# Performance work log

Hardware: AMD Instinct MI355X
Metric: run time of the kernel (lower is better)

Reference implementation:

```python
import jax, jax.numpy as jnp
import numpy as np

EPS = 1e-8


def setup_inputs() -> dict:
    key = jax.random.key(0)
    x = jax.random.normal(key, (16384, 1024), dtype=jnp.float32)
    return {"x": x}


def reference(x) -> jnp.ndarray:
    # L2 normalize along feature dim (torch F.normalize: x / max(||x||, eps))
    norm = jnp.linalg.norm(x, axis=-1, keepdims=True)
    xn = x / jnp.maximum(norm, EPS)

    n = xn.shape[0]
    # full pairwise cosine similarity [N, N]
    dot = xn @ xn.T
    # mask self-similarity on the diagonal
    ii = jnp.arange(n)
    dot = dot.at[ii, ii].set(-1.0)
    # nearest neighbor per row
    index = jnp.argmax(dot, axis=1)

    # torch PairwiseDistance(p=2, eps=1e-8): ||x1 - x2 + eps||_2
    diff = xn - xn[index] + EPS
    distances = jnp.linalg.norm(diff, axis=-1)

    loss = -jnp.mean(jnp.log(distances + EPS))
    return loss
```

## Files before the change

kernel.cpp:

```cpp
#include <hip/hip_runtime.h>
#include <math.h>

#define N 16384
#define D 1024
#define EPSF 1e-8f
#define QSCALE 448.0f
#define NPAIRS 2080
#define PANB 262144

typedef __attribute__((ext_vector_type(4))) int i32x4;
typedef unsigned int u32;
typedef unsigned long long u64;

#define LDS_Bb 65536
#define LDS_TOT 131088

__device__ __forceinline__ void gload_lds16(const void* g, void* l) {
  __builtin_amdgcn_global_load_lds(
      (const __attribute__((address_space(1))) u32*)g,
      (__attribute__((address_space(3))) u32*)l, 16, 0, 0);
}

__device__ __forceinline__ u64 maxu64(u64 x, u64 y) { return x > y ? x : y; }

__device__ __forceinline__ void decode_pair(int t, int& a, int& b) {
  int aa = (int)((129.0 - sqrt(129.0 * 129.0 - 8.0 * (double)t)) * 0.5);
  if (aa < 0) aa = 0;
  if (aa > 63) aa = 63;
  while (((aa + 1) * 64 - ((aa + 1) * aa) / 2) <= t) ++aa;
  while ((aa * 64 - (aa * (aa - 1)) / 2) > t) --aa;
  a = aa;
  b = aa + (t - (aa * 64 - (aa * (aa - 1)) / 2));
}


__global__ __launch_bounds__(256) void k_normalize(
    const float* __restrict__ x, signed char* __restrict__ xq,
    float* __restrict__ norms, u64* __restrict__ best, int* __restrict__ ctr) {
  const int w = threadIdx.x >> 6, lane = threadIdx.x & 63;
  const int i = blockIdx.x * 4 + w;
  if (threadIdx.x < 4) best[(size_t)blockIdx.x * 4 + threadIdx.x] = 0;
  if (blockIdx.x == 0 && threadIdx.x == 0) *ctr = 0;
  const float4* xi = (const float4*)(x + (size_t)i * D);
  float4 v[4];
  float s = 0.f;
#pragma unroll
  for (int t = 0; t < 4; ++t) {
    v[t] = xi[lane + t * 64];
    s += v[t].x * v[t].x + v[t].y * v[t].y + v[t].z * v[t].z + v[t].w * v[t].w;
  }
#pragma unroll
  for (int sh = 32; sh; sh >>= 1) s += __shfl_xor(s, sh, 64);
  const float nrm = sqrtf(s);
  if (lane == 0) norms[i] = nrm;
  const float qs = QSCALE / fmaxf(nrm, EPSF);
  u32* xo = (u32*)(xq + (size_t)i * D);
#pragma unroll
  for (int t = 0; t < 4; ++t) {
    const int q0 = __float2int_rn(fminf(fmaxf(v[t].x * qs, -127.f), 127.f));
    const int q1 = __float2int_rn(fminf(fmaxf(v[t].y * qs, -127.f), 127.f));
    const int q2 = __float2int_rn(fminf(fmaxf(v[t].z * qs, -127.f), 127.f));
    const int q3 = __float2int_rn(fminf(fmaxf(v[t].w * qs, -127.f), 127.f));
    xo[lane + t * 64] = (u32)(q0 & 0xff) | ((u32)(q1 & 0xff) << 8) |
                        ((u32)(q2 & 0xff) << 16) | ((u32)(q3 & 0xff) << 24);
  }
}


#define SG(gaddr, daddr) \
  gload_lds16(xqB + (gaddr) + srcLane, lds + (daddr) + w * 1024)

#define KT1(K_)                                                                \
  {                                                                            \
    __builtin_amdgcn_s_barrier();                                              \
    asm volatile("" ::: "memory");                                             \
    if ((K_) < 13) {                                                           \
      const size_t aG = aPan + (size_t)(((K_) + 3) * 64);                      \
      const size_t bG = bPan + (size_t)(((K_) + 3) * 64);                      \
      SG(aG, (((K_) + 3) & 3) * 16384);                                        \
      SG(aG + 131072, (((K_) + 3) & 3) * 16384 + 8192);                        \
      SG(bG, LDS_Bb + (((K_) + 3) & 3) * 16384);                               \
      SG(bG + 131072, LDS_Bb + (((K_) + 3) & 3) * 16384 + 8192);               \
    } else if (hasNext) {                                                      \
      const size_t aG = aPanN + (size_t)(((K_)-13) * 64);                      \
      const size_t bG = bPanN + (size_t)(((K_)-13) * 64);                      \
      SG(aG, (((K_) + 3) & 3) * 16384);                                        \
      SG(aG + 131072, (((K_) + 3) & 3) * 16384 + 8192);                        \
      SG(bG, LDS_Bb + (((K_) + 3) & 3) * 16384);                               \
      SG(bG + 131072, LDS_Bb + (((K_) + 3) & 3) * 16384 + 8192);               \
    }                                                                          \
    i32x4 aa[4], bb[4];                                                        \
    _Pragma("unroll") for (int m = 0; m < 4; ++m) aa[m] =                      \
        *(const i32x4*)(lds + ((K_)&3) * 16384 + aOff[m]);                     \
    _Pragma("unroll") for (int n = 0; n < 4; ++n) bb[n] =                      \
        *(const i32x4*)(lds + LDS_Bb + ((K_)&3) * 16384 + bOff[n]);            \
    __builtin_amdgcn_s_setprio(1);                                             \
    _Pragma("unroll") for (int m = 0; m < 4; ++m)                              \
      _Pragma("unroll") for (int n = 0; n < 4; ++n)                            \
        acc[m][n] = __builtin_amdgcn_mfma_i32_16x16x64_i8(aa[m], bb[n],        \
                                                          acc[m][n], 0, 0, 0); \
    __builtin_amdgcn_s_setprio(0);                                             \
    _Pragma("unroll") for (int n = 0; n < 4; ++n) bb[n] =                      \
        *(const i32x4*)(lds + LDS_Bb + ((K_)&3) * 16384 + bOff[4 + n]);        \
    __builtin_amdgcn_s_setprio(1);                                             \
    _Pragma("unroll") for (int m = 0; m < 4; ++m)                              \
      _Pragma("unroll") for (int n = 0; n < 4; ++n)                            \
        acc[m][4 + n] = __builtin_amdgcn_mfma_i32_16x16x64_i8(                 \
            aa[m], bb[n], acc[m][4 + n], 0, 0, 0);                             \
    __builtin_amdgcn_s_setprio(0);                                             \
    asm volatile("s_waitcnt vmcnt(8)" ::: "memory");                           \
  }

__global__ __launch_bounds__(512, 2) void k_argmax(
    const signed char* __restrict__ xq, u64* __restrict__ best,
    int* __restrict__ ctr) {
  extern __shared__ char lds[];
  int* s_next = (int*)(lds + 131072);
  const char* xqB = (const char*)xq;
  const int tid = (int)threadIdx.x, lane = tid & 63, w = tid >> 6;
  const int wr = w >> 1, wc = w & 1;

  int aOff[4], bOff[8];
  const int q = lane >> 4, li = lane & 15;
#pragma unroll
  for (int m = 0; m < 4; ++m) {
    const int rr = wr * 64 + m * 16 + li;
    const int line = rr >> 1;
    aOff[m] = line * 128 + ((((rr & 1) << 6) | (q << 4)) ^ ((line & 7) << 4));
  }
#pragma unroll
  for (int nf = 0; nf < 8; ++nf) {
    const int rr = wc * 128 + nf * 16 + li;
    const int line = rr >> 1;
    bOff[nf] = line * 128 + ((((rr & 1) << 6) | (q << 4)) ^ ((line & 7) << 4));
  }
  const int posx = (lane & 7) ^ (lane >> 3);
  const int rrl = ((w * 8 + (lane >> 3)) << 1) | (posx >> 2);
  const int srcLane = rrl * 1024 + (posx & 3) * 16;

  const int rB2 = wr * 64 + (q << 2);
  const int cB2 = wc * 128 + li;

  if (tid == 0) {
    s_next[0] = atomicAdd(ctr, 1);
    s_next[1] = atomicAdd(ctr, 1);
  }
  __syncthreads();
  int pcur = s_next[0], pnext = s_next[1];
  __syncthreads();
  if (pcur >= NPAIRS) return;

  int a, b;
  decode_pair(pcur, a, b);
  size_t aPan = (size_t)a * PANB, bPan = (size_t)b * PANB;
  for (int p = 0; p < 3; ++p) {
    SG(aPan + (size_t)(p * 64), p * 16384);
    SG(aPan + (size_t)(p * 64) + 131072, p * 16384 + 8192);
    SG(bPan + (size_t)(p * 64), LDS_Bb + p * 16384);
    SG(bPan + (size_t)(p * 64) + 131072, LDS_Bb + p * 16384 + 8192);
  }
  asm volatile("s_waitcnt vmcnt(8)" ::: "memory");

  int par = 0;
  i32x4 acc[4][8];
  while (true) {
    const bool hasNext = (pnext < NPAIRS);
    int an = 0, bn = 0;
    if (hasNext) decode_pair(pnext, an, bn);
    const size_t aPanN = (size_t)an * PANB, bPanN = (size_t)bn * PANB;
    if (tid == 0) s_next[par] = atomicAdd(ctr, 1);

#pragma unroll
    for (int m = 0; m < 4; ++m)
#pragma unroll
      for (int n = 0; n < 8; ++n) acc[m][n] = (i32x4){0, 0, 0, 0};

    KT1(0); KT1(1); KT1(2); KT1(3);
    KT1(4); KT1(5); KT1(6); KT1(7);
    KT1(8); KT1(9); KT1(10); KT1(11);
    KT1(12); KT1(13); KT1(14); KT1(15);

    const int aBase = a * 256, colBase = b * 256;
#pragma unroll
    for (int m = 0; m < 4; ++m)
#pragma unroll
      for (int r = 0; r < 4; ++r) {
        const int rl = rB2 + m * 16 + r;
        int pm = (int)0x80000000;
        if (a == b) {
#pragma unroll
          for (int nf = 0; nf < 8; ++nf) {
            int pv = (int)(((u32)acc[m][nf][r] << 3) | (u32)nf);
            if (rl == cB2 + nf * 16) pv = (int)0x80000000;
            pm = pm > pv ? pm : pv;
          }
        } else {
#pragma unroll
          for (int nf = 0; nf < 8; ++nf) {
            const int pv = (int)(((u32)acc[m][nf][r] << 3) | (u32)nf);
            pm = pm > pv ? pm : pv;
          }
        }
        const u32 mono = (u32)(pm >> 3) ^ 0x80000000u;
        u64 p = ((u64)mono << 32) | (u32)(colBase + cB2 + ((pm & 7) << 4));
#pragma unroll
        for (int sh = 1; sh < 16; sh <<= 1)
          p = maxu64(p, __shfl_xor(p, sh, 64));
        if (li == 0) atomicMax(best + (aBase + rl), p);
      }

    if (a != b) {
#pragma unroll
      for (int nf = 0; nf < 8; ++nf) {
        int pv = (int)0x80000000;
#pragma unroll
        for (int m = 0; m < 4; ++m)
#pragma unroll
          for (int r = 0; r < 4; ++r) {
            const int c =
                (int)(((u32)acc[m][nf][r] << 6) | (u32)(m * 16 + q * 4 + r));
            pv = pv > c ? pv : c;
          }
        {
          const int o1 = __shfl_xor(pv, 16, 64);
          pv = pv > o1 ? pv : o1;
          const int o2 = __shfl_xor(pv, 32, 64);
          pv = pv > o2 ? pv : o2;
        }
        if (q == 0) {
          const int dot = pv >> 6;
          const int grow = aBase + wr * 64 + (pv & 63);
          const u64 pk = ((u64)((u32)dot ^ 0x80000000u) << 32) | (u32)grow;
          atomicMax(best + (colBase + cB2 + nf * 16), pk);
        }
      }
    }

    if (!hasNext) break;
    const int pnn = s_next[par];
    pcur = pnext;
    a = an; b = bn;
    aPan = aPanN; bPan = bPanN;
    pnext = pnn;
    par ^= 1;
  }
}


__global__ __launch_bounds__(256) void k_dist(
    const float* __restrict__ x, const float* __restrict__ norms,
    const u64* __restrict__ best, float* __restrict__ logd) {
  const int w = threadIdx.x >> 6, lane = threadIdx.x & 63;
  const int i = blockIdx.x * 4 + w;
  const u64 p = best[i];
  const int j = (int)(p & 0xffffffffu);
  const float invi = 1.f / fmaxf(norms[i], EPSF);
  const float invj = 1.f / fmaxf(norms[j], EPSF);
  const float4* xi = (const float4*)(x + (size_t)i * D);
  const float4* xj = (const float4*)(x + (size_t)j * D);
  float s = 0.f;
#pragma unroll
  for (int t = 0; t < 4; ++t) {
    const float4 av = xi[lane + t * 64], bv = xj[lane + t * 64];
    float d;
    d = av.x * invi - bv.x * invj + EPSF; s += d * d;
    d = av.y * invi - bv.y * invj + EPSF; s += d * d;
    d = av.z * invi - bv.z * invj + EPSF; s += d * d;
    d = av.w * invi - bv.w * invj + EPSF; s += d * d;
  }
#pragma unroll
  for (int sh = 32; sh; sh >>= 1) s += __shfl_xor(s, sh, 64);
  if (lane == 0) logd[i] = logf(sqrtf(s) + EPSF);
}


__global__ __launch_bounds__(256) void k_final(const float* __restrict__ logd,
                                               float* __restrict__ out) {
  __shared__ double red[256];
  double s = 0.0;
  for (int i = threadIdx.x; i < N; i += 256) s += (double)logd[i];
  red[threadIdx.x] = s;
  __syncthreads();
  for (int sh = 128; sh; sh >>= 1) {
    if ((int)threadIdx.x < sh) red[threadIdx.x] += red[threadIdx.x + sh];
    __syncthreads();
  }
  if (threadIdx.x == 0) out[0] = (float)(-red[0] / (double)N);
}


extern "C" void kernel_launch(void* const* d_in, const int* in_sizes, int n_in,
                              void* d_out, int out_size, void* d_ws,
                              size_t ws_size, hipStream_t stream) {
  const float* x = (const float*)d_in[0];
  float* out = (float*)d_out;
  char* ws = (char*)d_ws;

  signed char* xq = (signed char*)ws;
  float* norms = (float*)(ws + 16777216);
  u64* best = (u64*)(ws + 16842752);
  float* logd = (float*)(ws + 16973824);
  int* ctr = (int*)(ws + 17039360);

  k_normalize<<<N / 4, 256, 0, stream>>>(x, xq, norms, best, ctr);
  k_argmax<<<256, 512, LDS_TOT, stream>>>(xq, best, ctr);
  k_dist<<<N / 4, 256, 0, stream>>>(x, norms, best, logd);
  k_final<<<1, 256, 0, stream>>>(logd, out);
}
```

Measured before the change: 252.9 us.

## Load A operand directly from global via transposed int8 copy, deepen B LDS ring

The normalize kernel now also writes a transposed, MFMA-fragment-ordered copy of the quantized matrix. The argmax kernel reads A fragments straight from global memory into registers instead of staging them through LDS. B alone uses the freed LDS as an 8-slot ring with a 4-tile prefetch distance, and barriers run once per group of four k-tiles with a full vmcnt(0) wait. This cuts LDS traffic and barrier count, at the cost of extra workspace, scattered 4-byte transposed writes in normalize, and global-load latency on A that is exposed directly to the MFMAs.

Measured after the change: 279.1 us. 10.4% more time.

```diff
diff --git a/kernel.cpp b/kernel.cpp
--- a/kernel.cpp
+++ b/kernel.cpp
@@ -7,12 +7,12 @@
 #define QSCALE 448.0f
 #define NPAIRS 2080
 #define PANB 262144
+#define GRANB 262144
 
 typedef __attribute__((ext_vector_type(4))) int i32x4;
 typedef unsigned int u32;
 typedef unsigned long long u64;
 
-#define LDS_Bb 65536
 #define LDS_TOT 131088
 
 __device__ __forceinline__ void gload_lds16(const void* g, void* l) {
@@ -36,7 +36,8 @@
 
 __global__ __launch_bounds__(256) void k_normalize(
     const float* __restrict__ x, signed char* __restrict__ xq,
-    float* __restrict__ norms, u64* __restrict__ best, int* __restrict__ ctr) {
+    signed char* __restrict__ xqT, float* __restrict__ norms,
+    u64* __restrict__ best, int* __restrict__ ctr) {
   const int w = threadIdx.x >> 6, lane = threadIdx.x & 63;
   const int i = blockIdx.x * 4 + w;
   if (threadIdx.x < 4) best[(size_t)blockIdx.x * 4 + threadIdx.x] = 0;
@@ -55,79 +56,95 @@
   if (lane == 0) norms[i] = nrm;
   const float qs = QSCALE / fmaxf(nrm, EPSF);
   u32* xo = (u32*)(xq + (size_t)i * D);
+  u32* xoT = (u32*)xqT;
 #pragma unroll
   for (int t = 0; t < 4; ++t) {
     const int q0 = __float2int_rn(fminf(fmaxf(v[t].x * qs, -127.f), 127.f));
     const int q1 = __float2int_rn(fminf(fmaxf(v[t].y * qs, -127.f), 127.f));
     const int q2 = __float2int_rn(fminf(fmaxf(v[t].z * qs, -127.f), 127.f));
     const int q3 = __float2int_rn(fminf(fmaxf(v[t].w * qs, -127.f), 127.f));
-    xo[lane + t * 64] = (u32)(q0 & 0xff) | ((u32)(q1 & 0xff) << 8) |
-                        ((u32)(q2 & 0xff) << 16) | ((u32)(q3 & 0xff) << 24);
-  }
-}
-
-
-#define SG(gaddr, daddr) \
+    const u32 val = (u32)(q0 & 0xff) | ((u32)(q1 & 0xff) << 8) |
+                    ((u32)(q2 & 0xff) << 16) | ((u32)(q3 & 0xff) << 24);
+    const int wrd = lane + t * 64;
+    xo[wrd] = val;
+    xoT[((size_t)(wrd >> 2) * 16384 + (u32)i) * 4 + (wrd & 3)] = val;
+  }
+}
+
+
+#define SGB(gaddr, daddr) \
   gload_lds16(xqB + (gaddr) + srcLane, lds + (daddr) + w * 1024)
 
-#define KT1(K_)                                                                \
+#define TILE(T_)                                                               \
+  {                                                                            \
+    const char* aT = xqTB + aRowB + (size_t)((T_)*4) * GRANB;                  \
+    const i32x4 aa0 = *(const i32x4*)(aT);                                     \
+    const i32x4 aa1 = *(const i32x4*)(aT + 256);                               \
+    const i32x4 aa2 = *(const i32x4*)(aT + 512);                               \
+    const i32x4 aa3 = *(const i32x4*)(aT + 768);                               \
+    if ((T_) < 12) {                                                           \
+      const size_t bG = bPan + (size_t)(((T_) + 4) * 64);                      \
+      SGB(bG, (((T_) + 4) & 7) * 16384);                                       \
+      SGB(bG + 131072, (((T_) + 4) & 7) * 16384 + 8192);                       \
+    } else if (hasNext) {                                                      \
+      const size_t bG = bPanN + (size_t)(((T_)-12) * 64);                      \
+      SGB(bG, (((T_) + 4) & 7) * 16384);                                       \
+      SGB(bG + 131072, (((T_) + 4) & 7) * 16384 + 8192);                       \
+    }                                                                          \
+    i32x4 bb[4];                                                               \
+    _Pragma("unroll") for (int n = 0; n < 4; ++n) bb[n] =                      \
+        *(const i32x4*)(lds + ((T_)&7) * 16384 + bOff[n]);                     \
+    __builtin_amdgcn_s_setprio(1);                                             \
+    _Pragma("unroll") for (int n = 0; n < 4; ++n) {                            \
+      acc[0][n] = __builtin_amdgcn_mfma_i32_16x16x64_i8(aa0, bb[n], acc[0][n], \
+                                                        0, 0, 0);              \
+      acc[1][n] = __builtin_amdgcn_mfma_i32_16x16x64_i8(aa1, bb[n], acc[1][n], \
+                                                        0, 0, 0);              \
+      acc[2][n] = __builtin_amdgcn_mfma_i32_16x16x64_i8(aa2, bb[n], acc[2][n], \
+                                                        0, 0, 0);              \
+      acc[3][n] = __builtin_amdgcn_mfma_i32_16x16x64_i8(aa3, bb[n], acc[3][n], \
+                                                        0, 0, 0);              \
+    }                                                                          \
+    __builtin_amdgcn_s_setprio(0);                                             \
+    _Pragma("unroll") for (int n = 0; n < 4; ++n) bb[n] =                      \
+        *(const i32x4*)(lds + ((T_)&7) * 16384 + bOff[4 + n]);                 \
+    __builtin_amdgcn_s_setprio(1);                                             \
+    _Pragma("unroll") for (int n = 0; n < 4; ++n) {                            \
+      acc[0][4 + n] = __builtin_amdgcn_mfma_i32_16x16x64_i8(                   \
+          aa0, bb[n], acc[0][4 + n], 0, 0, 0);                                 \
+      acc[1][4 + n] = __builtin_amdgcn_mfma_i32_16x16x64_i8(                   \
+          aa1, bb[n], acc[1][4 + n], 0, 0, 0);                                 \
+      acc[2][4 + n] = __builtin_amdgcn_mfma_i32_16x16x64_i8(                   \
+          aa2, bb[n], acc[2][4 + n], 0, 0, 0);                                 \
+      acc[3][4 + n] = __builtin_amdgcn_mfma_i32_16x16x64_i8(                   \
+          aa3, bb[n], acc[3][4 + n], 0, 0, 0);                                 \
+    }                                                                          \
+    __builtin_amdgcn_s_setprio(0);                                             \
+  }
+
+#define GROUP(G_)                                                              \
   {                                                                            \
     __builtin_amdgcn_s_barrier();                                              \
     asm volatile("" ::: "memory");                                             \
-    if ((K_) < 13) {                                                           \
-      const size_t aG = aPan + (size_t)(((K_) + 3) * 64);                      \
-      const size_t bG = bPan + (size_t)(((K_) + 3) * 64);                      \
-      SG(aG, (((K_) + 3) & 3) * 16384);                                        \
-      SG(aG + 131072, (((K_) + 3) & 3) * 16384 + 8192);                        \
-      SG(bG, LDS_Bb + (((K_) + 3) & 3) * 16384);                               \
-      SG(bG + 131072, LDS_Bb + (((K_) + 3) & 3) * 16384 + 8192);               \
-    } else if (hasNext) {                                                      \
-      const size_t aG = aPanN + (size_t)(((K_)-13) * 64);                      \
-      const size_t bG = bPanN + (size_t)(((K_)-13) * 64);                      \
-      SG(aG, (((K_) + 3) & 3) * 16384);                                        \
-      SG(aG + 131072, (((K_) + 3) & 3) * 16384 + 8192);                        \
-      SG(bG, LDS_Bb + (((K_) + 3) & 3) * 16384);                               \
-      SG(bG + 131072, LDS_Bb + (((K_) + 3) & 3) * 16384 + 8192);               \
-    }                                                                          \
-    i32x4 aa[4], bb[4];                                                        \
-    _Pragma("unroll") for (int m = 0; m < 4; ++m) aa[m] =                      \
-        *(const i32x4*)(lds + ((K_)&3) * 16384 + aOff[m]);                     \
-    _Pragma("unroll") for (int n = 0; n < 4; ++n) bb[n] =                      \
-        *(const i32x4*)(lds + LDS_Bb + ((K_)&3) * 16384 + bOff[n]);            \
-    __builtin_amdgcn_s_setprio(1);                                             \
-    _Pragma("unroll") for (int m = 0; m < 4; ++m)                              \
-      _Pragma("unroll") for (int n = 0; n < 4; ++n)                            \
-        acc[m][n] = __builtin_amdgcn_mfma_i32_16x16x64_i8(aa[m], bb[n],        \
-                                                          acc[m][n], 0, 0, 0); \
-    __builtin_amdgcn_s_setprio(0);                                             \
-    _Pragma("unroll") for (int n = 0; n < 4; ++n) bb[n] =                      \
-        *(const i32x4*)(lds + LDS_Bb + ((K_)&3) * 16384 + bOff[4 + n]);        \
-    __builtin_amdgcn_s_setprio(1);                                             \
-    _Pragma("unroll") for (int m = 0; m < 4; ++m)                              \
-      _Pragma("unroll") for (int n = 0; n < 4; ++n)                            \
-        acc[m][4 + n] = __builtin_amdgcn_mfma_i32_16x16x64_i8(                 \
-            aa[m], bb[n], acc[m][4 + n], 0, 0, 0);                             \
-    __builtin_amdgcn_s_setprio(0);                                             \
-    asm volatile("s_waitcnt vmcnt(8)" ::: "memory");                           \
+    TILE(4 * (G_) + 0);                                                        \
+    TILE(4 * (G_) + 1);                                                        \
+    TILE(4 * (G_) + 2);                                                        \
+    TILE(4 * (G_) + 3);                                                        \
+    asm volatile("s_waitcnt vmcnt(0)" ::: "memory");                           \
   }
 
 __global__ __launch_bounds__(512, 2) void k_argmax(
-    const signed char* __restrict__ xq, u64* __restrict__ best,
-    int* __restrict__ ctr) {
+    const signed char* __restrict__ xq, const signed char* __restrict__ xqT,
+    u64* __restrict__ best, int* __restrict__ ctr) {
   extern __shared__ char lds[];
   int* s_next = (int*)(lds + 131072);
   const char* xqB = (const char*)xq;
+  const char* xqTB = (const char*)xqT;
   const int tid = (int)threadIdx.x, lane = tid & 63, w = tid >> 6;
   const int wr = w >> 1, wc = w & 1;
 
-  int aOff[4], bOff[8];
+  int bOff[8];
   const int q = lane >> 4, li = lane & 15;
-#pragma unroll
-  for (int m = 0; m < 4; ++m) {
-    const int rr = wr * 64 + m * 16 + li;
-    const int line = rr >> 1;
-    aOff[m] = line * 128 + ((((rr & 1) << 6) | (q << 4)) ^ ((line & 7) << 4));
-  }
 #pragma unroll
   for (int nf = 0; nf < 8; ++nf) {
     const int rr = wc * 128 + nf * 16 + li;
@@ -152,14 +169,12 @@
 
   int a, b;
   decode_pair(pcur, a, b);
-  size_t aPan = (size_t)a * PANB, bPan = (size_t)b * PANB;
-  for (int p = 0; p < 3; ++p) {
-    SG(aPan + (size_t)(p * 64), p * 16384);
-    SG(aPan + (size_t)(p * 64) + 131072, p * 16384 + 8192);
-    SG(bPan + (size_t)(p * 64), LDS_Bb + p * 16384);
-    SG(bPan + (size_t)(p * 64) + 131072, LDS_Bb + p * 16384 + 8192);
-  }
-  asm volatile("s_waitcnt vmcnt(8)" ::: "memory");
+  size_t bPan = (size_t)b * PANB;
+  for (int p = 0; p < 4; ++p) {
+    SGB(bPan + (size_t)(p * 64), p * 16384);
+    SGB(bPan + (size_t)(p * 64) + 131072, p * 16384 + 8192);
+  }
+  asm volatile("s_waitcnt vmcnt(0)" ::: "memory");
 
   int par = 0;
   i32x4 acc[4][8];
@@ -167,18 +182,20 @@
     const bool hasNext = (pnext < NPAIRS);
     int an = 0, bn = 0;
     if (hasNext) decode_pair(pnext, an, bn);
-    const size_t aPanN = (size_t)an * PANB, bPanN = (size_t)bn * PANB;
+    const size_t bPanN = (size_t)bn * PANB;
     if (tid == 0) s_next[par] = atomicAdd(ctr, 1);
+    const size_t aRowB =
+        (size_t)q * GRANB + (size_t)(a * 256 + wr * 64 + li) * 16;
 
 #pragma unroll
     for (int m = 0; m < 4; ++m)
 #pragma unroll
       for (int n = 0; n < 8; ++n) acc[m][n] = (i32x4){0, 0, 0, 0};
 
-    KT1(0); KT1(1); KT1(2); KT1(3);
-    KT1(4); KT1(5); KT1(6); KT1(7);
-    KT1(8); KT1(9); KT1(10); KT1(11);
-    KT1(12); KT1(13); KT1(14); KT1(15);
+    GROUP(0)
+    GROUP(1)
+    GROUP(2)
+    GROUP(3)
 
     const int aBase = a * 256, colBase = b * 256;
 #pragma unroll
@@ -239,8 +256,9 @@
     if (!hasNext) break;
     const int pnn = s_next[par];
     pcur = pnext;
-    a = an; b = bn;
-    aPan = aPanN; bPan = bPanN;
+    a = an;
+    b = bn;
+    bPan = bPanN;
     pnext = pnn;
     par ^= 1;
   }
@@ -297,13 +315,14 @@
   char* ws = (char*)d_ws;
 
   signed char* xq = (signed char*)ws;
-  float* norms = (float*)(ws + 16777216);
-  u64* best = (u64*)(ws + 16842752);
-  float* logd = (float*)(ws + 16973824);
-  int* ctr = (int*)(ws + 17039360);
-
-  k_normalize<<<N / 4, 256, 0, stream>>>(x, xq, norms, best, ctr);
-  k_argmax<<<256, 512, LDS_TOT, stream>>>(xq, best, ctr);
+  signed char* xqT = (signed char*)(ws + 16777216);
+  float* norms = (float*)(ws + 33554432);
+  u64* best = (u64*)(ws + 33619968);
+  float* logd = (float*)(ws + 33751040);
+  int* ctr = (int*)(ws + 33816576);
+
+  k_normalize<<<N / 4, 256, 0, stream>>>(x, xq, xqT, norms, best, ctr);
+  k_argmax<<<256, 512, LDS_TOT, stream>>>(xq, xqT, best, ctr);
   k_dist<<<N / 4, 256, 0, stream>>>(x, norms, best, logd);
   k_final<<<1, 256, 0, stream>>>(logd, out);
 }
```

## Statically partition tile pairs across blocks and pack argmax keys into 32-bit

Applied to the files above, without the earlier changes.

Replaces the atomic work-stealing counter with a static contiguous split of the 2080 upper-triangle tile pairs across 256 blocks. This removes the per-pair global atomic and the LDS handoff with its extra barriers. The 16-step unrolled K loop becomes a 4x4 loop that always issues prefetch loads, reloading the current panel on the last pair, so some redundant loads are issued. Row argmax now packs the biased dot and the column index into a single 32-bit int, so the intra-row shuffle reduction uses 32-bit shuffles instead of 64-bit ones. The static split can cause load imbalance since blocks get 8 or 9 pairs, but it keeps neighbouring panels within a block.

Result: faster. 217.3 us (-14.1%).

```diff
diff --git a/kernel.cpp b/kernel.cpp
--- a/kernel.cpp
+++ b/kernel.cpp
@@ -6,14 +6,16 @@
 #define EPSF 1e-8f
 #define QSCALE 448.0f
 #define NPAIRS 2080
+#define NBLK 256
 #define PANB 262144
+#define BIAS 16777216u
 
 typedef __attribute__((ext_vector_type(4))) int i32x4;
 typedef unsigned int u32;
 typedef unsigned long long u64;
 
 #define LDS_Bb 65536
-#define LDS_TOT 131088
+#define LDS_TOT 131072
 
 __device__ __forceinline__ void gload_lds16(const void* g, void* l) {
   __builtin_amdgcn_global_load_lds(
@@ -22,6 +24,7 @@
 }
 
 __device__ __forceinline__ u64 maxu64(u64 x, u64 y) { return x > y ? x : y; }
+__device__ __forceinline__ int maxi(int x, int y) { return x > y ? x : y; }
 
 __device__ __forceinline__ void decode_pair(int t, int& a, int& b) {
   int aa = (int)((129.0 - sqrt(129.0 * 129.0 - 8.0 * (double)t)) * 0.5);
@@ -36,11 +39,10 @@
 
 __global__ __launch_bounds__(256) void k_normalize(
     const float* __restrict__ x, signed char* __restrict__ xq,
-    float* __restrict__ norms, u64* __restrict__ best, int* __restrict__ ctr) {
+    float* __restrict__ norms, u64* __restrict__ best) {
   const int w = threadIdx.x >> 6, lane = threadIdx.x & 63;
   const int i = blockIdx.x * 4 + w;
   if (threadIdx.x < 4) best[(size_t)blockIdx.x * 4 + threadIdx.x] = 0;
-  if (blockIdx.x == 0 && threadIdx.x == 0) *ctr = 0;
   const float4* xi = (const float4*)(x + (size_t)i * D);
   float4 v[4];
   float s = 0.f;
@@ -67,33 +69,27 @@
 }
 
 
-#define SG(gaddr, daddr) \
+#define SGB(gaddr, daddr) \
   gload_lds16(xqB + (gaddr) + srcLane, lds + (daddr) + w * 1024)
 
-#define KT1(K_)                                                                \
+#define KT(C_)                                                                 \
   {                                                                            \
+    const int k_ = kq * 4 + (C_);                                              \
+    const int t_ = k_ + 3;                                                     \
+    const int kt_ = t_ & 15;                                                   \
+    const size_t aG = (t_ >= 16 ? aPanN : aPan) + (size_t)(kt_ * 64);          \
+    const size_t bG = (t_ >= 16 ? bPanN : bPan) + (size_t)(kt_ * 64);          \
     __builtin_amdgcn_s_barrier();                                              \
     asm volatile("" ::: "memory");                                             \
-    if ((K_) < 13) {                                                           \
-      const size_t aG = aPan + (size_t)(((K_) + 3) * 64);                      \
-      const size_t bG = bPan + (size_t)(((K_) + 3) * 64);                      \
-      SG(aG, (((K_) + 3) & 3) * 16384);                                        \
-      SG(aG + 131072, (((K_) + 3) & 3) * 16384 + 8192);                        \
-      SG(bG, LDS_Bb + (((K_) + 3) & 3) * 16384);                               \
-      SG(bG + 131072, LDS_Bb + (((K_) + 3) & 3) * 16384 + 8192);               \
-    } else if (hasNext) {                                                      \
-      const size_t aG = aPanN + (size_t)(((K_)-13) * 64);                      \
-      const size_t bG = bPanN + (size_t)(((K_)-13) * 64);                      \
-      SG(aG, (((K_) + 3) & 3) * 16384);                                        \
-      SG(aG + 131072, (((K_) + 3) & 3) * 16384 + 8192);                        \
-      SG(bG, LDS_Bb + (((K_) + 3) & 3) * 16384);                               \
-      SG(bG + 131072, LDS_Bb + (((K_) + 3) & 3) * 16384 + 8192);               \
-    }                                                                          \
+    SGB(aG, (((C_) + 3) & 3) * 16384);                                         \
+    SGB(aG + 131072, (((C_) + 3) & 3) * 16384 + 8192);                         \
+    SGB(bG, LDS_Bb + (((C_) + 3) & 3) * 16384);                                \
+    SGB(bG + 131072, LDS_Bb + (((C_) + 3) & 3) * 16384 + 8192);                \
     i32x4 aa[4], bb[4];                                                        \
     _Pragma("unroll") for (int m = 0; m < 4; ++m) aa[m] =                      \
-        *(const i32x4*)(lds + ((K_)&3) * 16384 + aOff[m]);                     \
+        *(const i32x4*)(lds + ((C_)&3) * 16384 + aOff[m]);                     \
     _Pragma("unroll") for (int n = 0; n < 4; ++n) bb[n] =                      \
-        *(const i32x4*)(lds + LDS_Bb + ((K_)&3) * 16384 + bOff[n]);            \
+        *(const i32x4*)(lds + LDS_Bb + ((C_)&3) * 16384 + bOff[n]);            \
     __builtin_amdgcn_s_setprio(1);                                             \
     _Pragma("unroll") for (int m = 0; m < 4; ++m)                              \
       _Pragma("unroll") for (int n = 0; n < 4; ++n)                            \
@@ -101,7 +97,7 @@
                                                           acc[m][n], 0, 0, 0); \
     __builtin_amdgcn_s_setprio(0);                                             \
     _Pragma("unroll") for (int n = 0; n < 4; ++n) bb[n] =                      \
-        *(const i32x4*)(lds + LDS_Bb + ((K_)&3) * 16384 + bOff[4 + n]);        \
+        *(const i32x4*)(lds + LDS_Bb + ((C_)&3) * 16384 + bOff[4 + n]);        \
     __builtin_amdgcn_s_setprio(1);                                             \
     _Pragma("unroll") for (int m = 0; m < 4; ++m)                              \
       _Pragma("unroll") for (int n = 0; n < 4; ++n)                            \
@@ -112,10 +108,8 @@
   }
 
 __global__ __launch_bounds__(512, 2) void k_argmax(
-    const signed char* __restrict__ xq, u64* __restrict__ best,
-    int* __restrict__ ctr) {
+    const signed char* __restrict__ xq, u64* __restrict__ best) {
   extern __shared__ char lds[];
-  int* s_next = (int*)(lds + 131072);
   const char* xqB = (const char*)xq;
   const int tid = (int)threadIdx.x, lane = tid & 63, w = tid >> 6;
   const int wr = w >> 1, wc = w & 1;
@@ -141,44 +135,42 @@
   const int rB2 = wr * 64 + (q << 2);
   const int cB2 = wc * 128 + li;
 
-  if (tid == 0) {
-    s_next[0] = atomicAdd(ctr, 1);
-    s_next[1] = atomicAdd(ctr, 1);
-  }
-  __syncthreads();
-  int pcur = s_next[0], pnext = s_next[1];
-  __syncthreads();
-  if (pcur >= NPAIRS) return;
-
+  const int p0 = ((int)blockIdx.x * NPAIRS) / NBLK;
+  const int p1 = (((int)blockIdx.x + 1) * NPAIRS) / NBLK;
   int a, b;
-  decode_pair(pcur, a, b);
+  decode_pair(p0, a, b);
   size_t aPan = (size_t)a * PANB, bPan = (size_t)b * PANB;
-  for (int p = 0; p < 3; ++p) {
-    SG(aPan + (size_t)(p * 64), p * 16384);
-    SG(aPan + (size_t)(p * 64) + 131072, p * 16384 + 8192);
-    SG(bPan + (size_t)(p * 64), LDS_Bb + p * 16384);
-    SG(bPan + (size_t)(p * 64) + 131072, LDS_Bb + p * 16384 + 8192);
+
+  for (int pp = 0; pp < 3; ++pp) {
+    SGB(aPan + (size_t)(pp * 64), pp * 16384);
+    SGB(aPan + (size_t)(pp * 64) + 131072, pp * 16384 + 8192);
+    SGB(bPan + (size_t)(pp * 64), LDS_Bb + pp * 16384);
+    SGB(bPan + (size_t)(pp * 64) + 131072, LDS_Bb + pp * 16384 + 8192);
   }
   asm volatile("s_waitcnt vmcnt(8)" ::: "memory");
 
-  int par = 0;
   i32x4 acc[4][8];
-  while (true) {
-    const bool hasNext = (pnext < NPAIRS);
-    int an = 0, bn = 0;
-    if (hasNext) decode_pair(pnext, an, bn);
-    const size_t aPanN = (size_t)an * PANB, bPanN = (size_t)bn * PANB;
-    if (tid == 0) s_next[par] = atomicAdd(ctr, 1);
+  for (int p = p0; p < p1; ++p) {
+    int an = a, bn = b + 1;
+    if (bn == 64) {
+      an = a + 1;
+      bn = an;
+    }
+    const bool lastp = (p == p1 - 1);
+    const size_t aPanN = lastp ? aPan : (size_t)an * PANB;
+    const size_t bPanN = lastp ? bPan : (size_t)bn * PANB;
 
 #pragma unroll
     for (int m = 0; m < 4; ++m)
 #pragma unroll
       for (int n = 0; n < 8; ++n) acc[m][n] = (i32x4){0, 0, 0, 0};
 
-    KT1(0); KT1(1); KT1(2); KT1(3);
-    KT1(4); KT1(5); KT1(6); KT1(7);
-    KT1(8); KT1(9); KT1(10); KT1(11);
-    KT1(12); KT1(13); KT1(14); KT1(15);
+    for (int kq = 0; kq < 4; ++kq) {
+      KT(0)
+      KT(1)
+      KT(2)
+      KT(3)
+    }
 
     const int aBase = a * 256, colBase = b * 256;
 #pragma unroll
@@ -186,63 +178,60 @@
 #pragma unroll
       for (int r = 0; r < 4; ++r) {
         const int rl = rB2 + m * 16 + r;
-        int pm = (int)0x80000000;
+        int pk = 0;
         if (a == b) {
 #pragma unroll
           for (int nf = 0; nf < 8; ++nf) {
-            int pv = (int)(((u32)acc[m][nf][r] << 3) | (u32)nf);
-            if (rl == cB2 + nf * 16) pv = (int)0x80000000;
-            pm = pm > pv ? pm : pv;
+            int v = (int)((((u32)acc[m][nf][r] + BIAS) << 7) |
+                          (u32)((nf << 4) | li));
+            if (rl == cB2 + nf * 16) v = 0;
+            pk = maxi(pk, v);
           }
         } else {
 #pragma unroll
           for (int nf = 0; nf < 8; ++nf) {
-            const int pv = (int)(((u32)acc[m][nf][r] << 3) | (u32)nf);
-            pm = pm > pv ? pm : pv;
+            const int v = (int)((((u32)acc[m][nf][r] + BIAS) << 7) |
+                                (u32)((nf << 4) | li));
+            pk = maxi(pk, v);
           }
         }
-        const u32 mono = (u32)(pm >> 3) ^ 0x80000000u;
-        u64 p = ((u64)mono << 32) | (u32)(colBase + cB2 + ((pm & 7) << 4));
-#pragma unroll
-        for (int sh = 1; sh < 16; sh <<= 1)
-          p = maxu64(p, __shfl_xor(p, sh, 64));
-        if (li == 0) atomicMax(best + (aBase + rl), p);
+#pragma unroll
+        for (int sh = 1; sh < 16; sh <<= 1) pk = maxi(pk, __shfl_xor(pk, sh, 64));
+        if (li == 0) {
+          const int dot = (int)((((u32)pk) >> 7) - BIAS);
+          const int col = colBase + wc * 128 + (pk & 127);
+          const u64 key = ((u64)((u32)dot ^ 0x80000000u) << 32) | (u32)col;
+          atomicMax(best + (aBase + rl), key);
+        }
       }
 
     if (a != b) {
 #pragma unroll
       for (int nf = 0; nf < 8; ++nf) {
-        int pv = (int)0x80000000;
+        int pk = 0;
 #pragma unroll
         for (int m = 0; m < 4; ++m)
 #pragma unroll
           for (int r = 0; r < 4; ++r) {
-            const int c =
-                (int)(((u32)acc[m][nf][r] << 6) | (u32)(m * 16 + q * 4 + r));
-            pv = pv > c ? pv : c;
+            const int v = (int)((((u32)acc[m][nf][r] + BIAS) << 6) |
+                                (u32)(m * 16 + q * 4 + r));
+            pk = maxi(pk, v);
           }
-        {
-          const int o1 = __shfl_xor(pv, 16, 64);
-          pv = pv > o1 ? pv : o1;
-          const int o2 = __shfl_xor(pv, 32, 64);
-          pv = pv > o2 ? pv : o2;
-        }
+        pk = maxi(pk, __shfl_xor(pk, 16, 64));
+        pk = maxi(pk, __shfl_xor(pk, 32, 64));
         if (q == 0) {
-          const int dot = pv >> 6;
-          const int grow = aBase + wr * 64 + (pv & 63);
-          const u64 pk = ((u64)((u32)dot ^ 0x80000000u) << 32) | (u32)grow;
-          atomicMax(best + (colBase + cB2 + nf * 16), pk);
+          const int dot = (int)((((u32)pk) >> 6) - BIAS);
+          const int grow = aBase + wr * 64 + (pk & 63);
+          const u64 key = ((u64)((u32)dot ^ 0x80000000u) << 32) | (u32)grow;
+          atomicMax(best + (colBase + cB2 + nf * 16), key);
         }
       }
     }
 
-    if (!hasNext) break;
-    const int pnn = s_next[par];
-    pcur = pnext;
-    a = an; b = bn;
-    aPan = aPanN; bPan = bPanN;
-    pnext = pnn;
-    par ^= 1;
+    a = an;
+    b = bn;
+    aPan = (size_t)a * PANB;
+    bPan = (size_t)b * PANB;
   }
 }
 
@@ -300,10 +289,9 @@
   float* norms = (float*)(ws + 16777216);
   u64* best = (u64*)(ws + 16842752);
   float* logd = (float*)(ws + 16973824);
-  int* ctr = (int*)(ws + 17039360);
-
-  k_normalize<<<N / 4, 256, 0, stream>>>(x, xq, norms, best, ctr);
-  k_argmax<<<256, 512, LDS_TOT, stream>>>(xq, best, ctr);
+
+  k_normalize<<<N / 4, 256, 0, stream>>>(x, xq, norms, best);
+  k_argmax<<<NBLK, 512, LDS_TOT, stream>>>(xq, best);
   k_dist<<<N / 4, 256, 0, stream>>>(x, norms, best, logd);
   k_final<<<1, 256, 0, stream>>>(logd, out);
 }
```
